# Performance work log

Hardware: AMD Instinct MI355X
Metric: run time of the kernel (lower is better)

Reference implementation:

```python
import jax, jax.numpy as jnp
import numpy as np

N_NODES = 50000
N_EDGES = 600000
F_IN = 128
F_OUT = 128


def setup_inputs() -> dict:
    key = jax.random.key(0)
    k1, k2, k3, k4 = jax.random.split(key, 4)
    x = jax.random.normal(k1, (N_NODES, F_IN), dtype=jnp.float32)
    edge_index = jax.random.randint(k2, (2, N_EDGES), 0, N_NODES, dtype=jnp.int64)
    # Linear weights stored as [in, out] so out = h @ W + b
    scale = 1.0 / np.sqrt(F_IN)
    W_l = jax.random.uniform(k3, (F_IN, F_OUT), jnp.float32, -scale, scale)
    W_r = jax.random.uniform(k4, (F_IN, F_OUT), jnp.float32, -scale, scale)
    b_l = jnp.zeros((F_OUT,), jnp.float32)
    b_r = jnp.zeros((F_OUT,), jnp.float32)
    return {"x": x, "edge_index": edge_index, "W_l": W_l, "b_l": b_l, "W_r": W_r, "b_r": b_r}


def reference(x, edge_index, W_l, b_l, W_r, b_r):
    num_nodes = x.shape[0]
    src, dst = edge_index[0], edge_index[1]
    # P2_Gather: source node features per edge  [E, F]
    x_j = x[src]
    # P3_ScatterAdd: sum over incoming edges per destination node  [N, F]
    sum_agg = jax.ops.segment_sum(x_j, dst, num_segments=num_nodes)
    # P3_ScatterAdd_Count: in-degree per node  [N]
    count = jax.ops.segment_sum(jnp.ones_like(dst, dtype=x.dtype), dst,
                                num_segments=num_nodes)
    # P4_ElewiseDiv: mean aggregation (avoid div-by-zero for isolated nodes)
    mean_agg = sum_agg / jnp.maximum(count, 1.0)[:, None]
    # P1_Matmul_Dual + P5_ElewiseAct
    out = mean_agg @ W_l + b_l + x @ W_r + b_r
    return jax.nn.relu(out)
```

## Files before the change

### kernel.cpp

```cpp
#include <hip/hip_runtime.h>

#define NN 50000
#define NE 600000
#define FD 128
#define MAXD 64

using short8  = __attribute__((ext_vector_type(8))) short;
using ushort8 = __attribute__((ext_vector_type(8))) unsigned short;
using f32x4   = __attribute__((ext_vector_type(4))) float;

__device__ __forceinline__ unsigned short f2bf(float f) {
    unsigned int u = __float_as_uint(f);
    return (unsigned short)((u + 0x7FFFu + ((u >> 16) & 1u)) >> 16);
}
__device__ __forceinline__ float bf2f(unsigned short u) {
    return __uint_as_float(((unsigned int)u) << 16);
}

#define OFF_DEG   0
#define OFF_SLOT  200192
#define OFF_XB    6600192
#define OFF_WBT   19400192
#define WS_NEED   (19400192 + 65536)

#define NXB 3125
#define NWB 16
#define NZ  25

__global__ __launch_bounds__(256) void prep_k(const float* __restrict__ x,
                                              const float* __restrict__ Wl,
                                              const float* __restrict__ Wr,
                                              unsigned short* __restrict__ xb,
                                              unsigned short* __restrict__ wbT,
                                              int* __restrict__ deg) {
    int b = blockIdx.x;
    if (b < NXB) {
        int i = b * 256 + threadIdx.x;
        const float4* p = reinterpret_cast<const float4*>(x) + (size_t)i * 2;
        float4 a = p[0], c = p[1];
        short8 r;
        r[0] = (short)f2bf(a.x); r[1] = (short)f2bf(a.y);
        r[2] = (short)f2bf(a.z); r[3] = (short)f2bf(a.w);
        r[4] = (short)f2bf(c.x); r[5] = (short)f2bf(c.y);
        r[6] = (short)f2bf(c.z); r[7] = (short)f2bf(c.w);
        reinterpret_cast<short8*>(xb)[i] = r;
    } else if (b < NXB + NWB) {
        int u = (b - NXB) * 256 + threadIdx.x;
        int col = u & 127;
        int kb  = (u >> 7) * 8;
        short8 r;
        #pragma unroll
        for (int j = 0; j < 8; ++j) {
            int k = kb + j;
            float w = (k < 128) ? Wl[(size_t)k * FD + col]
                                : Wr[(size_t)(k - 128) * FD + col];
            r[j] = (short)f2bf(w);
        }
        *reinterpret_cast<short8*>(&wbT[col * 256 + kb]) = r;
    } else {
        int i = (b - NXB - NWB) * 256 + threadIdx.x;
        int4 z = {0, 0, 0, 0};
        *reinterpret_cast<int4*>(deg + i * 8)     = z;
        *reinterpret_cast<int4*>(deg + i * 8 + 4) = z;
    }
}

__global__ __launch_bounds__(256) void scatter_slot_k(const int* __restrict__ ei,
                                                      int* __restrict__ deg,
                                                      unsigned short* __restrict__ slot) {
    int e0 = (blockIdx.x * 256 + threadIdx.x) * 4;
    if (e0 >= NE) return;
    int4 s = *reinterpret_cast<const int4*>(ei + e0);
    int4 d = *reinterpret_cast<const int4*>(ei + NE + e0);
    int p;
    p = atomicAdd(&deg[d.x], 1); if (p < MAXD) slot[(size_t)d.x * MAXD + p] = (unsigned short)s.x;
    p = atomicAdd(&deg[d.y], 1); if (p < MAXD) slot[(size_t)d.y * MAXD + p] = (unsigned short)s.y;
    p = atomicAdd(&deg[d.z], 1); if (p < MAXD) slot[(size_t)d.z * MAXD + p] = (unsigned short)s.z;
    p = atomicAdd(&deg[d.w], 1); if (p < MAXD) slot[(size_t)d.w * MAXD + p] = (unsigned short)s.w;
}

__global__ __launch_bounds__(512) void agg_gemm_k(
    const unsigned short* __restrict__ xb,
    const int* __restrict__ deg,
    const unsigned short* __restrict__ slot,
    const unsigned short* __restrict__ wbT,
    const float* __restrict__ bl, const float* __restrict__ br,
    float* __restrict__ out)
{
    __shared__ __align__(16) unsigned short meanS[64][136];
    __shared__ __align__(16) unsigned short Bt[128][72];

    const int tid   = threadIdx.x;
    const int lane  = tid & 63;
    const int wid   = tid >> 6;
    const int node0 = blockIdx.x * 64;

    {
        const int l  = tid & 15;
        const int ng = tid >> 4;
        #pragma unroll
        for (int nb = 0; nb < 2; ++nb) {
            int nl = nb * 32 + ng;
            int n  = node0 + nl;
            float a[8] = {0.f, 0.f, 0.f, 0.f, 0.f, 0.f, 0.f, 0.f};
            float inv = 0.f;
            if (n < NN) {
                int cnt = deg[n];
                int dc  = cnt < MAXD ? cnt : MAXD;
                const unsigned short* sp = slot + (size_t)n * MAXD;
                for (int e0 = 0; e0 < dc; e0 += 8) {
                    ushort8 q = *reinterpret_cast<const ushort8*>(sp + e0);
                    #pragma unroll
                    for (int j = 0; j < 8; ++j) {
                        bool m  = (e0 + j) < dc;
                        int  sj = m ? (int)q[j] : 0;
                        float w = m ? 1.0f : 0.0f;
                        short8 v = *reinterpret_cast<const short8*>(
                            xb + (size_t)sj * FD + l * 8);
                        #pragma unroll
                        for (int k = 0; k < 8; ++k)
                            a[k] = fmaf(w, bf2f((unsigned short)v[k]), a[k]);
                    }
                }
                inv = 1.0f / fmaxf((float)cnt, 1.0f);
            }
            short8 r;
            #pragma unroll
            for (int j = 0; j < 8; ++j) r[j] = (short)f2bf(a[j] * inv);
            *reinterpret_cast<short8*>(&meanS[nl][l * 8]) = r;
        }
    }
    __syncthreads();

    const int rowq   = wid & 3;
    const int colh   = wid >> 2;
    const int arow_l = rowq * 16 + (lane & 15);
    const int arow   = node0 + arow_l;
    const int kgrp   = (lane >> 4) * 8;
    const int scol   = tid & 127;
    const int kb0    = (tid >> 7) * 16;

    f32x4 acc[4];
    #pragma unroll
    for (int c = 0; c < 4; ++c) acc[c] = (f32x4){0.f, 0.f, 0.f, 0.f};

    #pragma unroll
    for (int kc = 0; kc < 4; ++kc) {
        if (kc) __syncthreads();
        *reinterpret_cast<short8*>(&Bt[scol][kb0]) =
            *reinterpret_cast<const short8*>(&wbT[scol * 256 + kc * 64 + kb0]);
        *reinterpret_cast<short8*>(&Bt[scol][kb0 + 8]) =
            *reinterpret_cast<const short8*>(&wbT[scol * 256 + kc * 64 + kb0 + 8]);
        __syncthreads();

        #pragma unroll
        for (int ks = 0; ks < 2; ++ks) {
            int k0l = ks * 32 + kgrp;
            int k0g = kc * 64 + k0l;
            short8 af = {0, 0, 0, 0, 0, 0, 0, 0};
            if (kc < 2) {
                af = *reinterpret_cast<const short8*>(&meanS[arow_l][k0g]);
            } else if (arow < NN) {
                af = *reinterpret_cast<const short8*>(xb + (size_t)arow * FD + (k0g - 128));
            }
            #pragma unroll
            for (int c = 0; c < 4; ++c) {
                short8 bf = *reinterpret_cast<const short8*>(
                    &Bt[colh * 64 + c * 16 + (lane & 15)][k0l]);
                acc[c] = __builtin_amdgcn_mfma_f32_16x16x32_bf16(af, bf, acc[c], 0, 0, 0);
            }
        }
    }

    const int rbase = node0 + rowq * 16 + ((lane >> 4) << 2);
    #pragma unroll
    for (int c = 0; c < 4; ++c) {
        int col = colh * 64 + c * 16 + (lane & 15);
        float bsum_ = bl[col] + br[col];
        #pragma unroll
        for (int r = 0; r < 4; ++r) {
            int gr = rbase + r;
            if (gr < NN) {
                float v = acc[c][r] + bsum_;
                out[(size_t)gr * FD + col] = v > 0.f ? v : 0.f;
            }
        }
    }
}

#define FOFF_ROWPTR 0
#define FOFF_CURSOR 200064
#define FOFF_CSR    400128
#define FOFF_BSUM   2800384

__global__ __launch_bounds__(256) void hist_k(const int* __restrict__ ei,
                                              int* __restrict__ deg) {
    int e = blockIdx.x * 256 + threadIdx.x;
    if (e < NE) atomicAdd(&deg[ei[NE + e]], 1);
}

__global__ __launch_bounds__(256) void scan1_k(const int* __restrict__ deg,
                                               int* __restrict__ row_ptr,
                                               int* __restrict__ bsum) {
    __shared__ int ws[4];
    int i = blockIdx.x * 256 + threadIdx.x;
    int v = (i < NN) ? deg[i] : 0;
    int lane = threadIdx.x & 63, wid = threadIdx.x >> 6;
    int val = v;
    #pragma unroll
    for (int off = 1; off < 64; off <<= 1) {
        int t = __shfl_up(val, off);
        if (lane >= off) val += t;
    }
    if (lane == 63) ws[wid] = val;
    __syncthreads();
    int pre = 0;
    #pragma unroll
    for (int w = 0; w < 4; ++w) if (w < wid) pre += ws[w];
    val += pre;
    if (i < NN) row_ptr[i + 1] = val;
    if (threadIdx.x == 255) bsum[blockIdx.x] = val;
}

__global__ __launch_bounds__(256) void scan23_k(int* __restrict__ row_ptr,
                                                int* __restrict__ cursor,
                                                const int* __restrict__ bsum) {
    __shared__ int wsum[4];
    int t = threadIdx.x;
    int v = (t < (int)blockIdx.x) ? bsum[t] : 0;
    int lane = t & 63, wid = t >> 6;
    int val = v;
    #pragma unroll
    for (int off = 32; off; off >>= 1) val += __shfl_xor(val, off);
    if (lane == 0) wsum[wid] = val;
    __syncthreads();
    int offset = wsum[0] + wsum[1] + wsum[2] + wsum[3];
    int i = blockIdx.x * 256 + t;
    if (i == 0) row_ptr[0] = 0;
    if (i < NN) {
        int incl = row_ptr[i + 1] + offset;
        int d = cursor[i];
        row_ptr[i + 1] = incl;
        cursor[i] = incl - d;
    }
}

__global__ __launch_bounds__(256) void fill_k(const int* __restrict__ ei,
                                              int* __restrict__ cursor,
                                              int* __restrict__ csr_src) {
    int e = blockIdx.x * 256 + threadIdx.x;
    if (e < NE) {
        int s = ei[e];
        int d = ei[NE + e];
        int p = atomicAdd(&cursor[d], 1);
        csr_src[p] = s;
    }
}

__global__ __launch_bounds__(256) void agg_f32_k(const float* __restrict__ x,
                                                 const int* __restrict__ row_ptr,
                                                 const int* __restrict__ csr_src,
                                                 float* __restrict__ out) {
    int t = blockIdx.x * 256 + threadIdx.x;
    int n = t >> 5;
    if (n >= NN) return;
    int l = t & 31;
    int beg = row_ptr[n], end = row_ptr[n + 1];
    float4 a0 = make_float4(0.f, 0.f, 0.f, 0.f);
    float4 a1 = make_float4(0.f, 0.f, 0.f, 0.f);
    const float4* x4 = reinterpret_cast<const float4*>(x);
    int e = beg;
    for (; e + 1 < end; e += 2) {
        int s0 = csr_src[e], s1 = csr_src[e + 1];
        float4 v0 = x4[(size_t)s0 * 32 + l];
        float4 v1 = x4[(size_t)s1 * 32 + l];
        a0.x += v0.x; a0.y += v0.y; a0.z += v0.z; a0.w += v0.w;
        a1.x += v1.x; a1.y += v1.y; a1.z += v1.z; a1.w += v1.w;
    }
    if (e < end) {
        int s0 = csr_src[e];
        float4 v0 = x4[(size_t)s0 * 32 + l];
        a0.x += v0.x; a0.y += v0.y; a0.z += v0.z; a0.w += v0.w;
    }
    float inv = 1.0f / fmaxf((float)(end - beg), 1.0f);
    float4 r;
    r.x = (a0.x + a1.x) * inv; r.y = (a0.y + a1.y) * inv;
    r.z = (a0.z + a1.z) * inv; r.w = (a0.w + a1.w) * inv;
    reinterpret_cast<float4*>(out)[(size_t)n * 32 + l] = r;
}

__global__ __launch_bounds__(256) void gemm_f32_k(
    float* __restrict__ out, const float* __restrict__ x,
    const float* __restrict__ Wl, const float* __restrict__ bl,
    const float* __restrict__ Wr, const float* __restrict__ br)
{
    __shared__ __align__(16) unsigned short Btf[128][136];
    const int tid  = threadIdx.x;
    const int lane = tid & 63;
    const int wid  = tid >> 6;
    const int row0 = blockIdx.x * 64 + wid * 16;
    const int arow = row0 + (lane & 15);
    const bool rok = arow < NN;
    const int kgrp = (lane >> 4) * 8;
    f32x4 acc[8];
    #pragma unroll
    for (int c = 0; c < 8; ++c) acc[c] = (f32x4){0.f, 0.f, 0.f, 0.f};
    const int scol  = tid & 127;
    const int shalf = tid >> 7;
    #pragma unroll
    for (int p = 0; p < 2; ++p) {
        if (p) __syncthreads();
        const float* W = p ? Wr : Wl;
        #pragma unroll
        for (int kk = 0; kk < 64; kk += 8) {
            int kb = shalf * 64 + kk;
            short8 w;
            #pragma unroll
            for (int j = 0; j < 8; ++j) w[j] = (short)f2bf(W[(size_t)(kb + j) * FD + scol]);
            *reinterpret_cast<short8*>(&Btf[scol][kb]) = w;
        }
        __syncthreads();
        #pragma unroll
        for (int ks = 0; ks < 4; ++ks) {
            int k0 = ks * 32 + kgrp;
            short8 af = {0, 0, 0, 0, 0, 0, 0, 0};
            if (rok) {
                const float* ap = (p ? x : out) + (size_t)arow * FD + k0;
                float4 v0 = *reinterpret_cast<const float4*>(ap);
                float4 v1 = *reinterpret_cast<const float4*>(ap + 4);
                af[0] = (short)f2bf(v0.x); af[1] = (short)f2bf(v0.y);
                af[2] = (short)f2bf(v0.z); af[3] = (short)f2bf(v0.w);
                af[4] = (short)f2bf(v1.x); af[5] = (short)f2bf(v1.y);
                af[6] = (short)f2bf(v1.z); af[7] = (short)f2bf(v1.w);
            }
            #pragma unroll
            for (int c = 0; c < 8; ++c) {
                short8 bf = *reinterpret_cast<const short8*>(&Btf[c * 16 + (lane & 15)][k0]);
                acc[c] = __builtin_amdgcn_mfma_f32_16x16x32_bf16(af, bf, acc[c], 0, 0, 0);
            }
        }
    }
    const int rbase = row0 + ((lane >> 4) << 2);
    #pragma unroll
    for (int c = 0; c < 8; ++c) {
        int col = c * 16 + (lane & 15);
        float bsum_ = bl[col] + br[col];
        #pragma unroll
        for (int r = 0; r < 4; ++r) {
            int gr = rbase + r;
            if (gr < NN) {
                float v = acc[c][r] + bsum_;
                out[(size_t)gr * FD + col] = v > 0.f ? v : 0.f;
            }
        }
    }
}

extern "C" void kernel_launch(void* const* d_in, const int* in_sizes, int n_in,
                              void* d_out, int out_size, void* d_ws, size_t ws_size,
                              hipStream_t stream) {
    const float* x  = (const float*)d_in[0];
    const int*   ei = (const int*)d_in[1];
    const float* Wl = (const float*)d_in[2];
    const float* bl = (const float*)d_in[3];
    const float* Wr = (const float*)d_in[4];
    const float* br = (const float*)d_in[5];
    float* out = (float*)d_out;
    char* ws = (char*)d_ws;

    if (ws_size >= WS_NEED) {
        int* deg = (int*)(ws + OFF_DEG);
        unsigned short* slot = (unsigned short*)(ws + OFF_SLOT);
        unsigned short* xb   = (unsigned short*)(ws + OFF_XB);
        unsigned short* wbT  = (unsigned short*)(ws + OFF_WBT);

        prep_k        <<<NXB + NWB + NZ, 256, 0, stream>>>(x, Wl, Wr, xb, wbT, deg);
        scatter_slot_k<<<(NE / 4 + 255) / 256, 256, 0, stream>>>(ei, deg, slot);
        agg_gemm_k    <<<(NN + 63) / 64, 512, 0, stream>>>(xb, deg, slot, wbT,
                                                           bl, br, out);
    } else {
        int* row_ptr = (int*)(ws + FOFF_ROWPTR);
        int* cursor  = (int*)(ws + FOFF_CURSOR);
        int* csr_src = (int*)(ws + FOFF_CSR);
        int* bsum    = (int*)(ws + FOFF_BSUM);

        hipMemsetAsync(cursor, 0, (size_t)NN * sizeof(int), stream);
        hist_k  <<<(NE + 255) / 256, 256, 0, stream>>>(ei, cursor);
        scan1_k <<<196, 256, 0, stream>>>(cursor, row_ptr, bsum);
        scan23_k<<<196, 256, 0, stream>>>(row_ptr, cursor, bsum);
        fill_k  <<<(NE + 255) / 256, 256, 0, stream>>>(ei, cursor, csr_src);
        agg_f32_k<<<(NN * 32 + 255) / 256, 256, 0, stream>>>(x, row_ptr, csr_src, out);
        gemm_f32_k<<<(NN + 63) / 64, 256, 0, stream>>>(out, x, Wl, bl, Wr, br);
    }
}
```

Baseline: 83.80 us.

## Split fused gather+GEMM into separate gather and GEMM kernels

Unfuses the neighbor-mean aggregation from the MFMA GEMM kernel into a standalone gather kernel that writes a bf16 mean buffer to workspace, followed by a GEMM kernel that reads it back. The gather kernel uses small 256-thread blocks with an occupancy hint and an unmasked main loop with a masked tail, so the irregular gather can run at higher occupancy without being tied to the GEMM's shared memory and 512-thread blocks. The cost is an extra kernel launch plus a ~12.8MB write and read of the intermediate mean buffer, and a larger workspace requirement.

```diff
diff --git a/kernel.cpp b/kernel.cpp
--- a/kernel.cpp
+++ b/kernel.cpp
@@ -20,8 +20,9 @@
 #define OFF_DEG   0
 #define OFF_SLOT  200192
 #define OFF_XB    6600192
-#define OFF_WBT   19400192
-#define WS_NEED   (19400192 + 65536)
+#define OFF_MEANB 19400192
+#define OFF_WBT   32200192
+#define WS_NEED   (32200192 + 65536)
 
 #define NXB 3125
 #define NWB 16
@@ -79,58 +80,67 @@
     p = atomicAdd(&deg[d.w], 1); if (p < MAXD) slot[(size_t)d.w * MAXD + p] = (unsigned short)s.w;
 }
 
-__global__ __launch_bounds__(512) void agg_gemm_k(
+__global__ __launch_bounds__(256, 8) void gather_k(
     const unsigned short* __restrict__ xb,
     const int* __restrict__ deg,
     const unsigned short* __restrict__ slot,
+    unsigned short* __restrict__ meanb)
+{
+    int t = blockIdx.x * 256 + threadIdx.x;
+    int n = t >> 4;
+    if (n >= NN) return;
+    const int l = t & 15;
+
+    int cnt = deg[n];
+    int dc  = cnt < MAXD ? cnt : MAXD;
+    const unsigned short* sp = slot + (size_t)n * MAXD;
+
+    float a[8] = {0.f, 0.f, 0.f, 0.f, 0.f, 0.f, 0.f, 0.f};
+    int e0 = 0;
+    for (; e0 + 8 <= dc; e0 += 8) {
+        ushort8 q = *reinterpret_cast<const ushort8*>(sp + e0);
+        #pragma unroll
+        for (int j = 0; j < 8; ++j) {
+            short8 v = *reinterpret_cast<const short8*>(
+                xb + (size_t)(unsigned)q[j] * FD + l * 8);
+            #pragma unroll
+            for (int k = 0; k < 8; ++k) a[k] += bf2f((unsigned short)v[k]);
+        }
+    }
+    if (e0 < dc) {
+        ushort8 q = *reinterpret_cast<const ushort8*>(sp + e0);
+        #pragma unroll
+        for (int j = 0; j < 8; ++j) {
+            bool m  = (e0 + j) < dc;
+            int  sj = m ? (int)q[j] : 0;
+            float w = m ? 1.0f : 0.0f;
+            short8 v = *reinterpret_cast<const short8*>(
+                xb + (size_t)sj * FD + l * 8);
+            #pragma unroll
+            for (int k = 0; k < 8; ++k)
+                a[k] = fmaf(w, bf2f((unsigned short)v[k]), a[k]);
+        }
+    }
+    float inv = 1.0f / fmaxf((float)cnt, 1.0f);
+    short8 r;
+    #pragma unroll
+    for (int j = 0; j < 8; ++j) r[j] = (short)f2bf(a[j] * inv);
+    *reinterpret_cast<short8*>(meanb + (size_t)n * FD + l * 8) = r;
+}
+
+__global__ __launch_bounds__(512) void gemm_k(
+    const unsigned short* __restrict__ xb,
+    const unsigned short* __restrict__ meanb,
     const unsigned short* __restrict__ wbT,
     const float* __restrict__ bl, const float* __restrict__ br,
     float* __restrict__ out)
 {
-    __shared__ __align__(16) unsigned short meanS[64][136];
     __shared__ __align__(16) unsigned short Bt[128][72];
 
     const int tid   = threadIdx.x;
     const int lane  = tid & 63;
     const int wid   = tid >> 6;
     const int node0 = blockIdx.x * 64;
-
-    {
-        const int l  = tid & 15;
-        const int ng = tid >> 4;
-        #pragma unroll
-        for (int nb = 0; nb < 2; ++nb) {
-            int nl = nb * 32 + ng;
-            int n  = node0 + nl;
-            float a[8] = {0.f, 0.f, 0.f, 0.f, 0.f, 0.f, 0.f, 0.f};
-            float inv = 0.f;
-            if (n < NN) {
-                int cnt = deg[n];
-                int dc  = cnt < MAXD ? cnt : MAXD;
-                const unsigned short* sp = slot + (size_t)n * MAXD;
-                for (int e0 = 0; e0 < dc; e0 += 8) {
-                    ushort8 q = *reinterpret_cast<const ushort8*>(sp + e0);
-                    #pragma unroll
-                    for (int j = 0; j < 8; ++j) {
-                        bool m  = (e0 + j) < dc;
-                        int  sj = m ? (int)q[j] : 0;
-                        float w = m ? 1.0f : 0.0f;
-                        short8 v = *reinterpret_cast<const short8*>(
-                            xb + (size_t)sj * FD + l * 8);
-                        #pragma unroll
-                        for (int k = 0; k < 8; ++k)
-                            a[k] = fmaf(w, bf2f((unsigned short)v[k]), a[k]);
-                    }
-                }
-                inv = 1.0f / fmaxf((float)cnt, 1.0f);
-            }
-            short8 r;
-            #pragma unroll
-            for (int j = 0; j < 8; ++j) r[j] = (short)f2bf(a[j] * inv);
-            *reinterpret_cast<short8*>(&meanS[nl][l * 8]) = r;
-        }
-    }
-    __syncthreads();
 
     const int rowq   = wid & 3;
     const int colh   = wid >> 2;
@@ -158,10 +168,10 @@
             int k0l = ks * 32 + kgrp;
             int k0g = kc * 64 + k0l;
             short8 af = {0, 0, 0, 0, 0, 0, 0, 0};
-            if (kc < 2) {
-                af = *reinterpret_cast<const short8*>(&meanS[arow_l][k0g]);
-            } else if (arow < NN) {
-                af = *reinterpret_cast<const short8*>(xb + (size_t)arow * FD + (k0g - 128));
+            if (arow < NN) {
+                const unsigned short* base = (kc < 2) ? meanb : xb;
+                int off = (kc < 2) ? k0g : (k0g - 128);
+                af = *reinterpret_cast<const short8*>(base + (size_t)arow * FD + off);
             }
             #pragma unroll
             for (int c = 0; c < 4; ++c) {
@@ -370,14 +380,15 @@
 
     if (ws_size >= WS_NEED) {
         int* deg = (int*)(ws + OFF_DEG);
-        unsigned short* slot = (unsigned short*)(ws + OFF_SLOT);
-        unsigned short* xb   = (unsigned short*)(ws + OFF_XB);
-        unsigned short* wbT  = (unsigned short*)(ws + OFF_WBT);
+        unsigned short* slot  = (unsigned short*)(ws + OFF_SLOT);
+        unsigned short* xb    = (unsigned short*)(ws + OFF_XB);
+        unsigned short* meanb = (unsigned short*)(ws + OFF_MEANB);
+        unsigned short* wbT   = (unsigned short*)(ws + OFF_WBT);
 
         prep_k        <<<NXB + NWB + NZ, 256, 0, stream>>>(x, Wl, Wr, xb, wbT, deg);
         scatter_slot_k<<<(NE / 4 + 255) / 256, 256, 0, stream>>>(ei, deg, slot);
-        agg_gemm_k    <<<(NN + 63) / 64, 512, 0, stream>>>(xb, deg, slot, wbT,
-                                                           bl, br, out);
+        gather_k      <<<(NN * 16) / 256, 256, 0, stream>>>(xb, deg, slot, meanb);
+        gemm_k        <<<(NN + 63) / 64, 512, 0, stream>>>(xb, meanb, wbT, bl, br, out);
     } else {
         int* row_ptr = (int*)(ws + FOFF_ROWPTR);
         int* cursor  = (int*)(ws + FOFF_CURSOR);
```

New measurement: 87.47 us. 4.4% more time.
